# Kernel tuning notes

Hardware: AMD Instinct MI355X
Metric: run time of the kernel (lower is better)

Reference implementation:

```python
import jax, jax.numpy as jnp
import numpy as np

N_NODES = 100000  # number of graph nodes (adj is [N,N])


def setup_inputs() -> dict:
    key = jax.random.key(0)
    k1, k2, k3, k4 = jax.random.split(key, 4)
    E = 3200000
    D = 16
    row = jnp.sort(jax.random.randint(k1, (E,), 0, N_NODES, dtype=jnp.int32))
    col = jax.random.randint(k2, (E,), 0, N_NODES, dtype=jnp.int32)
    vals = jax.random.uniform(k3, (E,), dtype=jnp.float32)
    embeds = jax.random.normal(k4, (N_NODES, D), dtype=jnp.float32)
    return {"row": row, "col": col, "vals": vals, "embeds": embeds}


def reference(row, col, vals, embeds):
    # out = A @ embeds, A given in COO form: A[row[e], col[e]] = vals[e]
    # gather source features, scale by edge weight, scatter-add into rows
    msgs = vals[:, None] * embeds[col]  # [E, D]
    out = jax.ops.segment_sum(msgs, row, num_segments=N_NODES)  # [N, D]
    return out
```

## Files before the change

kernel.cpp:

```cpp
#include <hip/hip_runtime.h>
#include <hip/hip_fp16.h>


#define D 16
constexpr int BLOCK = 256;
constexpr int NPB = BLOCK / 4;
constexpr int SMEM_E = 3072;

typedef float f32x4 __attribute__((ext_vector_type(4)));
typedef int   i32x4 __attribute__((ext_vector_type(4)));
typedef unsigned int u32x2 __attribute__((ext_vector_type(2)));
typedef unsigned int u32x4 __attribute__((ext_vector_type(4)));

__device__ inline float2 h2f(unsigned int u) {
  union { unsigned int u; __half2 h; } cv;
  cv.u = u;
  return __half22float2(cv.h);
}

__global__ __launch_bounds__(BLOCK) void prep_kernel(
    const int* __restrict__ row, int E,
    const float* __restrict__ embeds, int N,
    int* __restrict__ row_ptr, __half* __restrict__ table) {
  const long long t = (long long)blockIdx.x * BLOCK + threadIdx.x;

  if (table != nullptr) {
    const long long nchunkA = (long long)N * 2;
    if (t < nchunkA) {
      const f32x4* src = (const f32x4*)embeds + t * 2;
      f32x4 a = __builtin_nontemporal_load(src);
      f32x4 b = __builtin_nontemporal_load(src + 1);
      union { __half2 h[4]; u32x4 u; } o;
      o.h[0] = __floats2half2_rn(a[0], a[1]);
      o.h[1] = __floats2half2_rn(a[2], a[3]);
      o.h[2] = __floats2half2_rn(b[0], b[1]);
      o.h[3] = __floats2half2_rn(b[2], b[3]);
      *((u32x4*)table + t) = o.u;
    }
  }

  const long long e = t * 4;
  if (e < E) {
    int prev = (e == 0) ? -1 : row[e - 1];
    const int cnt = (E - e >= 4) ? 4 : (int)(E - e);
    int r[4];
    if (cnt == 4) {
      i32x4 r4 = *(const i32x4*)(row + e);
      r[0] = r4[0]; r[1] = r4[1]; r[2] = r4[2]; r[3] = r4[3];
    } else {
      for (int k = 0; k < cnt; ++k) r[k] = row[e + k];
    }
    for (int k = 0; k < cnt; ++k) {
      for (int n = prev + 1; n <= r[k]; ++n) row_ptr[n] = (int)e + k;
      prev = r[k];
    }
    if (e + cnt == E) {
      for (int n = prev + 1; n <= N; ++n) row_ptr[n] = E;
    }
  }
}

__global__ __launch_bounds__(BLOCK) void gcn_gather_kernel(
    const int* __restrict__ col, const float* __restrict__ vals,
    const __half* __restrict__ table, const int* __restrict__ row_ptr,
    f32x4* __restrict__ out4, int N, int E) {
  __shared__ __align__(16) unsigned int s_meta[SMEM_E * 2];

  const int t = threadIdx.x;
  const int n0 = blockIdx.x * NPB;
  const int nEnd = (n0 + NPB < N) ? n0 + NPB : N;
  const int g = t >> 2;
  const int q = t & 3;
  const int node = n0 + g;
  const bool active = (node < nEnd);

  const int Wb = row_ptr[n0] & ~3;
  const int We = row_ptr[nEnd];

  const int beg = active ? row_ptr[node] : 0;
  const int end = active ? row_ptr[node + 1] : 0;
  const unsigned q8 = (unsigned)(q << 3);
  const char* tbl = (const char*)table;

  f32x4 acc = {0.f, 0.f, 0.f, 0.f};

  for (int W0 = Wb; W0 < We; W0 += SMEM_E) {
    const int cnt  = (SMEM_E < We - W0) ? SMEM_E : (We - W0);
    const int cntP = (cnt + 7) & ~7;
    __syncthreads();
    for (int i = t * 4; i < cntP; i += BLOCK * 4) {
      const int e = W0 + i;
      u32x4 lo, hi;
      if (e + 3 < E) {
        i32x4 c4 = *(const i32x4*)(col + e);
        f32x4 v4 = *(const f32x4*)(vals + e);
        lo = (u32x4){(unsigned)c4[0], __float_as_uint(v4[0]),
                     (unsigned)c4[1], __float_as_uint(v4[1])};
        hi = (u32x4){(unsigned)c4[2], __float_as_uint(v4[2]),
                     (unsigned)c4[3], __float_as_uint(v4[3])};
      } else {
        unsigned cc[4], vv[4];
        for (int k = 0; k < 4; ++k) {
          cc[k] = (e + k < E) ? (unsigned)col[e + k] : 0u;
          vv[k] = (e + k < E) ? __float_as_uint(vals[e + k]) : 0u;
        }
        lo = (u32x4){cc[0], vv[0], cc[1], vv[1]};
        hi = (u32x4){cc[2], vv[2], cc[3], vv[3]};
      }
      *(u32x4*)(s_meta + (size_t)i * 2)     = lo;
      *(u32x4*)(s_meta + (size_t)i * 2 + 4) = hi;
    }
    __syncthreads();

    const int gb = (beg > W0) ? beg : W0;
    const int ge = (end < W0 + cnt) ? end : (W0 + cnt);
    if (ge > gb) {
      const unsigned span = (unsigned)(ge - gb);
      const int e0 = W0 + ((gb - W0) & ~7);
      const int e1 = e0 + ((ge - e0 + 7) & ~7);
      for (int e = e0; e < e1; e += 8) {
        const int idx = (e - W0) * 2;
        u32x4 mA = *(const u32x4*)(s_meta + idx);
        u32x4 mB = *(const u32x4*)(s_meta + idx + 4);
        u32x4 mC = *(const u32x4*)(s_meta + idx + 8);
        u32x4 mD = *(const u32x4*)(s_meta + idx + 12);
        u32x2 g0 = *(const u32x2*)(tbl + (size_t)((mA[0] << 5) + q8));
        u32x2 g1 = *(const u32x2*)(tbl + (size_t)((mA[2] << 5) + q8));
        u32x2 g2 = *(const u32x2*)(tbl + (size_t)((mB[0] << 5) + q8));
        u32x2 g3 = *(const u32x2*)(tbl + (size_t)((mB[2] << 5) + q8));
        u32x2 g4 = *(const u32x2*)(tbl + (size_t)((mC[0] << 5) + q8));
        u32x2 g5 = *(const u32x2*)(tbl + (size_t)((mC[2] << 5) + q8));
        u32x2 g6 = *(const u32x2*)(tbl + (size_t)((mD[0] << 5) + q8));
        u32x2 g7 = *(const u32x2*)(tbl + (size_t)((mD[2] << 5) + q8));
#define EDGE(i, gg, vbits)                                            \
        {                                                             \
          float w = ((unsigned)(e + i - gb) < span)                   \
                        ? __uint_as_float(vbits) : 0.f;               \
          float2 lo2 = h2f(gg[0]), hi2 = h2f(gg[1]);                  \
          acc[0] = fmaf(w, lo2.x, acc[0]);                            \
          acc[1] = fmaf(w, lo2.y, acc[1]);                            \
          acc[2] = fmaf(w, hi2.x, acc[2]);                            \
          acc[3] = fmaf(w, hi2.y, acc[3]);                            \
        }
        EDGE(0, g0, mA[1])
        EDGE(1, g1, mA[3])
        EDGE(2, g2, mB[1])
        EDGE(3, g3, mB[3])
        EDGE(4, g4, mC[1])
        EDGE(5, g5, mC[3])
        EDGE(6, g6, mD[1])
        EDGE(7, g7, mD[3])
#undef EDGE
      }
    }
  }

  if (active) {
    __builtin_nontemporal_store(acc, out4 + (size_t)node * 4 + q);
  }
}

__global__ __launch_bounds__(BLOCK) void gcn_node_f32_kernel(
    const int* __restrict__ col, const float* __restrict__ vals,
    const f32x4* __restrict__ embeds4, const int* __restrict__ row_ptr,
    f32x4* __restrict__ out4, int N, int E) {
  const int t = blockIdx.x * BLOCK + threadIdx.x;
  const int node = t >> 2;
  const int q = t & 3;
  if (node >= N) return;
  const int beg = row_ptr[node];
  const int end = row_ptr[node + 1];
  f32x4 acc = {0.f, 0.f, 0.f, 0.f};
  for (int e = beg; e < end; ++e) {
    acc += vals[e] * embeds4[(long long)col[e] * 4 + q];
  }
  __builtin_nontemporal_store(acc, out4 + (long long)node * 4 + q);
}

extern "C" void kernel_launch(void* const* d_in, const int* in_sizes, int n_in,
                              void* d_out, int out_size, void* d_ws, size_t ws_size,
                              hipStream_t stream) {
  const int*   row    = (const int*)d_in[0];
  const int*   col    = (const int*)d_in[1];
  const float* vals   = (const float*)d_in[2];
  const float* embeds = (const float*)d_in[3];

  const int E = in_sizes[0];
  const int N = in_sizes[3] / D;

  const size_t rp_bytes = ((size_t)(N + 1) * 4 + 511) & ~(size_t)511;
  const size_t tbl_bytes = (size_t)N * D * sizeof(__half);
  const bool use_half = (ws_size >= rp_bytes + tbl_bytes) && (E >= 4);

  int*    row_ptr = (int*)d_ws;
  __half* table   = use_half ? (__half*)((char*)d_ws + rp_bytes) : nullptr;

  {
    long long chunksB = ((long long)E + 3) / 4;
    long long chunksA = use_half ? (long long)N * 2 : 0;
    long long threads = chunksB > chunksA ? chunksB : chunksA;
    int grid = (int)((threads + BLOCK - 1) / BLOCK);
    prep_kernel<<<grid, BLOCK, 0, stream>>>(row, E, embeds, N, row_ptr, table);
  }
  if (use_half) {
    int grid = (N + NPB - 1) / NPB;
    gcn_gather_kernel<<<grid, BLOCK, 0, stream>>>(
        col, vals, table, row_ptr, (f32x4*)d_out, N, E);
  } else {
    long long threads = (long long)N * 4;
    int grid = (int)((threads + BLOCK - 1) / BLOCK);
    gcn_node_f32_kernel<<<grid, BLOCK, 0, stream>>>(
        col, vals, (const f32x4*)embeds, row_ptr, (f32x4*)d_out, N, E);
  }
}
```

Measured before the change: 38.42 us.

## Software-pipeline gather loop with prefetched metadata and padded shared layout

Restructures the per-node gather loop into a software pipeline. Shared-memory metadata for the next two 8-edge groups is loaded ahead, and the table gathers for the next group are issued before the current group is consumed, with a sched_barrier keeping that order. The shared buffer gains padding (4 words per 64) to reduce bank conflicts, and the embeds loads in prep are no longer nontemporal. This aims to hide global gather latency, at the cost of higher register pressure that may lower occupancy.

```diff
diff --git a/kernel.cpp b/kernel.cpp
--- a/kernel.cpp
+++ b/kernel.cpp
@@ -4,7 +4,7 @@
 
 #define D 16
 constexpr int BLOCK = 256;
-constexpr int NPB = BLOCK / 4;
+constexpr int NPB = 64;
 constexpr int SMEM_E = 3072;
 
 typedef float f32x4 __attribute__((ext_vector_type(4)));
@@ -12,10 +12,11 @@
 typedef unsigned int u32x2 __attribute__((ext_vector_type(2)));
 typedef unsigned int u32x4 __attribute__((ext_vector_type(4)));
 
-__device__ inline float2 h2f(unsigned int u) {
-  union { unsigned int u; __half2 h; } cv;
-  cv.u = u;
-  return __half22float2(cv.h);
+__device__ __forceinline__ unsigned cvIdx(unsigned i) { return i + ((i >> 6) << 2); }
+
+__device__ __forceinline__ float2 h2f(unsigned u) {
+  union { unsigned u; __half2 h; } c; c.u = u;
+  return __half22float2(c.h);
 }
 
 __global__ __launch_bounds__(BLOCK) void prep_kernel(
@@ -25,11 +26,10 @@
   const long long t = (long long)blockIdx.x * BLOCK + threadIdx.x;
 
   if (table != nullptr) {
-    const long long nchunkA = (long long)N * 2;
-    if (t < nchunkA) {
+    if (t < (long long)N * 2) {
       const f32x4* src = (const f32x4*)embeds + t * 2;
-      f32x4 a = __builtin_nontemporal_load(src);
-      f32x4 b = __builtin_nontemporal_load(src + 1);
+      f32x4 a = src[0];
+      f32x4 b = src[1];
       union { __half2 h[4]; u32x4 u; } o;
       o.h[0] = __floats2half2_rn(a[0], a[1]);
       o.h[1] = __floats2half2_rn(a[2], a[3]);
@@ -60,27 +60,62 @@
   }
 }
 
-__global__ __launch_bounds__(BLOCK) void gcn_gather_kernel(
+__device__ __forceinline__ void ldmeta(const unsigned* __restrict__ s_cv,
+                                       unsigned i0, u32x4 M[4]) {
+  const unsigned ci = cvIdx(i0 * 2);
+  M[0] = *(const u32x4*)(s_cv + ci);
+  M[1] = *(const u32x4*)(s_cv + ci + 4);
+  M[2] = *(const u32x4*)(s_cv + ci + 8);
+  M[3] = *(const u32x4*)(s_cv + ci + 12);
+}
+
+__device__ __forceinline__ void gath(const char* __restrict__ tb,
+                                     const u32x4 M[4], unsigned q8, u32x2 G[8]) {
+  G[0] = *(const u32x2*)(tb + (size_t)(M[0][0] << 5) + q8);
+  G[1] = *(const u32x2*)(tb + (size_t)(M[0][2] << 5) + q8);
+  G[2] = *(const u32x2*)(tb + (size_t)(M[1][0] << 5) + q8);
+  G[3] = *(const u32x2*)(tb + (size_t)(M[1][2] << 5) + q8);
+  G[4] = *(const u32x2*)(tb + (size_t)(M[2][0] << 5) + q8);
+  G[5] = *(const u32x2*)(tb + (size_t)(M[2][2] << 5) + q8);
+  G[6] = *(const u32x2*)(tb + (size_t)(M[3][0] << 5) + q8);
+  G[7] = *(const u32x2*)(tb + (size_t)(M[3][2] << 5) + q8);
+}
+
+__device__ __forceinline__ void cons8(f32x4& acc, const u32x4 M[4],
+                                      const u32x2 G[8], int e, int gb,
+                                      unsigned span) {
+  const unsigned vv[8] = {M[0][1], M[0][3], M[1][1], M[1][3],
+                          M[2][1], M[2][3], M[3][1], M[3][3]};
+  #pragma unroll
+  for (int i = 0; i < 8; ++i) {
+    const float w = ((unsigned)(e + i - gb) < span) ? __uint_as_float(vv[i]) : 0.f;
+    const float2 lo = h2f(G[i][0]), hi = h2f(G[i][1]);
+    acc[0] = fmaf(w, lo.x, acc[0]);
+    acc[1] = fmaf(w, lo.y, acc[1]);
+    acc[2] = fmaf(w, hi.x, acc[2]);
+    acc[3] = fmaf(w, hi.y, acc[3]);
+  }
+}
+
+__global__ __launch_bounds__(BLOCK) void gcn_half_kernel(
     const int* __restrict__ col, const float* __restrict__ vals,
     const __half* __restrict__ table, const int* __restrict__ row_ptr,
     f32x4* __restrict__ out4, int N, int E) {
-  __shared__ __align__(16) unsigned int s_meta[SMEM_E * 2];
+  __shared__ __align__(16) unsigned s_cv[SMEM_E * 2 + (SMEM_E * 2 / 64) * 4];
 
   const int t = threadIdx.x;
   const int n0 = blockIdx.x * NPB;
   const int nEnd = (n0 + NPB < N) ? n0 + NPB : N;
   const int g = t >> 2;
-  const int q = t & 3;
+  const unsigned q8 = (unsigned)((t & 3) << 3);
   const int node = n0 + g;
   const bool active = (node < nEnd);
 
   const int Wb = row_ptr[n0] & ~3;
   const int We = row_ptr[nEnd];
-
   const int beg = active ? row_ptr[node] : 0;
   const int end = active ? row_ptr[node + 1] : 0;
-  const unsigned q8 = (unsigned)(q << 3);
-  const char* tbl = (const char*)table;
+  const char* tb = (const char*)table;
 
   f32x4 acc = {0.f, 0.f, 0.f, 0.f};
 
@@ -90,25 +125,25 @@
     __syncthreads();
     for (int i = t * 4; i < cntP; i += BLOCK * 4) {
       const int e = W0 + i;
-      u32x4 lo, hi;
+      unsigned c[4], v[4];
       if (e + 3 < E) {
         i32x4 c4 = *(const i32x4*)(col + e);
         f32x4 v4 = *(const f32x4*)(vals + e);
-        lo = (u32x4){(unsigned)c4[0], __float_as_uint(v4[0]),
-                     (unsigned)c4[1], __float_as_uint(v4[1])};
-        hi = (u32x4){(unsigned)c4[2], __float_as_uint(v4[2]),
-                     (unsigned)c4[3], __float_as_uint(v4[3])};
+        #pragma unroll
+        for (int k = 0; k < 4; ++k) {
+          c[k] = (unsigned)c4[k];
+          v[k] = __float_as_uint(v4[k]);
+        }
       } else {
-        unsigned cc[4], vv[4];
+        #pragma unroll
         for (int k = 0; k < 4; ++k) {
-          cc[k] = (e + k < E) ? (unsigned)col[e + k] : 0u;
-          vv[k] = (e + k < E) ? __float_as_uint(vals[e + k]) : 0u;
+          const bool ok = (e + k < E);
+          c[k] = ok ? (unsigned)col[e + k] : 0u;
+          v[k] = ok ? __float_as_uint(vals[e + k]) : 0u;
         }
-        lo = (u32x4){cc[0], vv[0], cc[1], vv[1]};
-        hi = (u32x4){cc[2], vv[2], cc[3], vv[3]};
       }
-      *(u32x4*)(s_meta + (size_t)i * 2)     = lo;
-      *(u32x4*)(s_meta + (size_t)i * 2 + 4) = hi;
+      *(u32x4*)(s_cv + cvIdx((unsigned)i * 2))     = (u32x4){c[0], v[0], c[1], v[1]};
+      *(u32x4*)(s_cv + cvIdx((unsigned)i * 2) + 4) = (u32x4){c[2], v[2], c[3], v[3]};
     }
     __syncthreads();
 
@@ -118,45 +153,31 @@
       const unsigned span = (unsigned)(ge - gb);
       const int e0 = W0 + ((gb - W0) & ~7);
       const int e1 = e0 + ((ge - e0 + 7) & ~7);
+      const int eL = e1 - 8;
+
+      u32x4 M0[4], M1[4], M2[4];
+      u32x2 G0[8], G1[8];
+      const int p1 = (e0 + 8 < eL) ? e0 + 8 : eL;
+      ldmeta(s_cv, (unsigned)(e0 - W0), M0);
+      ldmeta(s_cv, (unsigned)(p1 - W0), M1);
+      gath(tb, M0, q8, G0);
+
       for (int e = e0; e < e1; e += 8) {
-        const int idx = (e - W0) * 2;
-        u32x4 mA = *(const u32x4*)(s_meta + idx);
-        u32x4 mB = *(const u32x4*)(s_meta + idx + 4);
-        u32x4 mC = *(const u32x4*)(s_meta + idx + 8);
-        u32x4 mD = *(const u32x4*)(s_meta + idx + 12);
-        u32x2 g0 = *(const u32x2*)(tbl + (size_t)((mA[0] << 5) + q8));
-        u32x2 g1 = *(const u32x2*)(tbl + (size_t)((mA[2] << 5) + q8));
-        u32x2 g2 = *(const u32x2*)(tbl + (size_t)((mB[0] << 5) + q8));
-        u32x2 g3 = *(const u32x2*)(tbl + (size_t)((mB[2] << 5) + q8));
-        u32x2 g4 = *(const u32x2*)(tbl + (size_t)((mC[0] << 5) + q8));
-        u32x2 g5 = *(const u32x2*)(tbl + (size_t)((mC[2] << 5) + q8));
-        u32x2 g6 = *(const u32x2*)(tbl + (size_t)((mD[0] << 5) + q8));
-        u32x2 g7 = *(const u32x2*)(tbl + (size_t)((mD[2] << 5) + q8));
-#define EDGE(i, gg, vbits)                                            \
-        {                                                             \
-          float w = ((unsigned)(e + i - gb) < span)                   \
-                        ? __uint_as_float(vbits) : 0.f;               \
-          float2 lo2 = h2f(gg[0]), hi2 = h2f(gg[1]);                  \
-          acc[0] = fmaf(w, lo2.x, acc[0]);                            \
-          acc[1] = fmaf(w, lo2.y, acc[1]);                            \
-          acc[2] = fmaf(w, hi2.x, acc[2]);                            \
-          acc[3] = fmaf(w, hi2.y, acc[3]);                            \
-        }
-        EDGE(0, g0, mA[1])
-        EDGE(1, g1, mA[3])
-        EDGE(2, g2, mB[1])
-        EDGE(3, g3, mB[3])
-        EDGE(4, g4, mC[1])
-        EDGE(5, g5, mC[3])
-        EDGE(6, g6, mD[1])
-        EDGE(7, g7, mD[3])
-#undef EDGE
+        const int p2 = (e + 16 < eL) ? e + 16 : eL;
+        ldmeta(s_cv, (unsigned)(p2 - W0), M2);
+        gath(tb, M1, q8, G1);
+        __builtin_amdgcn_sched_barrier(0);
+        cons8(acc, M0, G0, e, gb, span);
+        #pragma unroll
+        for (int j = 0; j < 4; ++j) { M0[j] = M1[j]; M1[j] = M2[j]; }
+        #pragma unroll
+        for (int j = 0; j < 8; ++j) { G0[j] = G1[j]; }
       }
     }
   }
 
   if (active) {
-    __builtin_nontemporal_store(acc, out4 + (size_t)node * 4 + q);
+    __builtin_nontemporal_store(acc, out4 + (size_t)node * 4 + (t & 3));
   }
 }
 
@@ -188,9 +209,9 @@
   const int E = in_sizes[0];
   const int N = in_sizes[3] / D;
 
-  const size_t rp_bytes = ((size_t)(N + 1) * 4 + 511) & ~(size_t)511;
+  const size_t rp_bytes  = ((size_t)(N + 1) * 4 + 511) & ~(size_t)511;
   const size_t tbl_bytes = (size_t)N * D * sizeof(__half);
-  const bool use_half = (ws_size >= rp_bytes + tbl_bytes) && (E >= 4);
+  const bool use_half = (ws_size >= rp_bytes + tbl_bytes) && (E >= 8);
 
   int*    row_ptr = (int*)d_ws;
   __half* table   = use_half ? (__half*)((char*)d_ws + rp_bytes) : nullptr;
@@ -203,8 +224,8 @@
     prep_kernel<<<grid, BLOCK, 0, stream>>>(row, E, embeds, N, row_ptr, table);
   }
   if (use_half) {
-    int grid = (N + NPB - 1) / NPB;
-    gcn_gather_kernel<<<grid, BLOCK, 0, stream>>>(
+    const int grid = (N + NPB - 1) / NPB;
+    gcn_half_kernel<<<grid, BLOCK, 0, stream>>>(
         col, vals, table, row_ptr, (f32x4*)d_out, N, E);
   } else {
     long long threads = (long long)N * 4;
```

Result: slower. 40.58 us (+5.6%).
